# Kernel tuning notes

Measured on AMD Instinct MI355X. Metric: run time of the kernel, lower is better.

## Reference

```python
import jax, jax.numpy as jnp
import numpy as np

TAU = 1.0
NUM_CLASSES = 14
EDGE_W = 500.0
BODY_W = 200.0
LOSS_W = 1.0


def _cross_reduce(x, op, pad_val):
    """Apply op over the 3D 6-neighborhood cross (scipy default structure).
    x: bool [B, C, D, H, W]."""
    p = jnp.pad(x, ((0, 0), (0, 0), (1, 1), (1, 1), (1, 1)), constant_values=pad_val)
    r = p[:, :, 1:-1, 1:-1, 1:-1]
    r = op(r, p[:, :, :-2, 1:-1, 1:-1]); r = op(r, p[:, :, 2:, 1:-1, 1:-1])
    r = op(r, p[:, :, 1:-1, :-2, 1:-1]); r = op(r, p[:, :, 1:-1, 2:, 1:-1])
    r = op(r, p[:, :, 1:-1, 1:-1, :-2]); r = op(r, p[:, :, 1:-1, 1:-1, 2:])
    return r


def _edge_body_masks(gt_labels):
    # gt_labels: int [B, 1, D, H, W] -> bool masks [B, NUM_CLASSES, D, H, W]
    gt = gt_labels[:, 0]  # [B, D, H, W]
    onehot = gt[:, None] == jnp.arange(NUM_CLASSES, dtype=gt.dtype)[None, :, None, None, None]
    # binary_dilation ^ binary_erosion, both with border_value=0 (scipy default)
    dil = _cross_reduce(onehot, jnp.logical_or, False)
    ero = _cross_reduce(onehot, jnp.logical_and, False)
    edges = jnp.logical_xor(dil, ero)
    bodies = jnp.logical_and(jnp.logical_not(edges), onehot)
    # class 0 (background) masks are forced to zero in the original loop
    edges = edges.at[:, 0].set(False)
    bodies = bodies.at[:, 0].set(False)
    return edges, bodies


def _cwd(preds_S, preds_T):
    # ChannelWiseDivergence: per-(batch,channel) softmax over flattened spatial dims
    B, C = preds_S.shape[0], preds_S.shape[1]
    s = preds_S.reshape(B * C, -1) / TAU
    t = preds_T.reshape(B * C, -1) / TAU
    p_t = jax.nn.softmax(t, axis=-1)
    loss = jnp.sum(p_t * (jax.nn.log_softmax(t, axis=-1) - jax.nn.log_softmax(s, axis=-1)))
    return loss * (TAU ** 2) / (B * C)


def setup_inputs() -> dict:
    key = jax.random.key(0)
    k1, k2, k3 = jax.random.split(key, 3)
    B, C, D, H, W = 2, NUM_CLASSES, 96, 96, 96
    preds_S = jax.random.normal(k1, (B, C, D, H, W), dtype=jnp.float32)
    preds_T = jax.random.normal(k2, (B, C, D, H, W), dtype=jnp.float32)
    gt_labels = jax.random.randint(k3, (B, 1, D, H, W), 0, NUM_CLASSES, dtype=jnp.int64)
    return {"preds_S": preds_S, "preds_T": preds_T, "gt_labels": gt_labels}


def reference(preds_S, preds_T, gt_labels):
    B = preds_S.shape[0]
    edges, bodies = _edge_body_masks(gt_labels)
    me = edges.astype(preds_S.dtype)
    mb = bodies.astype(preds_S.dtype)
    loss_edges = _cwd(preds_S * me, preds_T * me) * LOSS_W * EDGE_W / B
    loss_bodies = _cwd(preds_S * mb, preds_T * mb) * LOSS_W * BODY_W / B
    return loss_edges, loss_bodies
```

## Files before the change

kernel.cpp:

```cpp
#include <hip/hip_runtime.h>
#include <math.h>

#define NCLS 14
#define DIMX 96
#define DIMXY (DIMX * DIMX)
#define NVOX (DIMX * DIMX * DIMX)
#define BATCH 2
#define ROWS (BATCH * NCLS)
#define TPB 256
#define VPT 2
#define CPB (TPB * 4 * VPT)
#define NBLK (NVOX / CPB)

__global__ __launch_bounds__(256) void mask_kernel(const int* __restrict__ gt,
                                                   unsigned* __restrict__ masks,
                                                   float* __restrict__ body_acc) {
    if (blockIdx.x == 0 && threadIdx.x < ROWS * 4) body_acc[threadIdx.x] = 0.f;
    int idx4 = blockIdx.x * 256 + threadIdx.x;
    if (idx4 >= BATCH * NVOX / 4) return;
    int v4 = idx4 * 4;
    int b = v4 / NVOX;
    int v = v4 - b * NVOX;
    int w = v % DIMX;
    int h = (v / DIMX) % DIMX;
    int d = v / DIMXY;
    const int* __restrict__ g = gt + (size_t)b * NVOX;

    int gc[4];
    { int4 t4 = *(const int4*)&g[v]; gc[0] = t4.x; gc[1] = t4.y; gc[2] = t4.z; gc[3] = t4.w; }
    bool hasU = h > 0, hasD = h < DIMX - 1, hasF = d > 0, hasB = d < DIMX - 1;
    bool hasL0 = w > 0;
    bool hasR3 = (w + 3) < DIMX - 1;
    int up[4], dn[4], fr[4], bk[4];
    if (hasU) { int4 t4 = *(const int4*)&g[v - DIMX];  up[0]=t4.x; up[1]=t4.y; up[2]=t4.z; up[3]=t4.w; }
    if (hasD) { int4 t4 = *(const int4*)&g[v + DIMX];  dn[0]=t4.x; dn[1]=t4.y; dn[2]=t4.z; dn[3]=t4.w; }
    if (hasF) { int4 t4 = *(const int4*)&g[v - DIMXY]; fr[0]=t4.x; fr[1]=t4.y; fr[2]=t4.z; fr[3]=t4.w; }
    if (hasB) { int4 t4 = *(const int4*)&g[v + DIMXY]; bk[0]=t4.x; bk[1]=t4.y; bk[2]=t4.z; bk[3]=t4.w; }
    int lf0 = hasL0 ? g[v - 1] : 0;
    int rt3 = hasR3 ? g[v + 4] : 0;

    unsigned res[4];
    #pragma unroll
    for (int j = 0; j < 4; ++j) {
        int c0 = gc[j];
        unsigned dil = 1u << c0;
        bool all = hasU && hasD && hasF && hasB;
        int  lf = (j == 0) ? lf0 : gc[j - 1]; bool hl = (j > 0) || hasL0;
        int  rt = (j == 3) ? rt3 : gc[j + 1]; bool hr = (j < 3) || hasR3;
        all = all && hl && hr;
        if (hl)   { dil |= 1u << lf;    all = all && (lf == c0); }
        if (hr)   { dil |= 1u << rt;    all = all && (rt == c0); }
        if (hasU) { dil |= 1u << up[j]; all = all && (up[j] == c0); }
        if (hasD) { dil |= 1u << dn[j]; all = all && (dn[j] == c0); }
        if (hasF) { dil |= 1u << fr[j]; all = all && (fr[j] == c0); }
        if (hasB) { dil |= 1u << bk[j]; all = all && (bk[j] == c0); }
        unsigned edge = dil & ~1u;
        if (all) edge &= ~(1u << c0);
        unsigned bodyc = (all && c0 != 0) ? (unsigned)c0 : 15u;
        res[j] = edge | (bodyc << 16);
    }
    *(uint4*)&masks[(size_t)v4] = make_uint4(res[0], res[1], res[2], res[3]);
}

__global__ __launch_bounds__(TPB) void cwd_kernel(const float* __restrict__ Sp,
                                                  const float* __restrict__ Tp,
                                                  const unsigned* __restrict__ masks,
                                                  float* __restrict__ partials,
                                                  float* __restrict__ body_acc) {
    int blk = blockIdx.x;
    int b = blk / NBLK;
    int chunk = blk - b * NBLK;
    const unsigned* __restrict__ mp = masks + (size_t)b * NVOX;
    const float* __restrict__ tb = Tp + (size_t)b * NCLS * NVOX;
    const float* __restrict__ sb = Sp + (size_t)b * NCLS * NVOX;
    int base = chunk * CPB + (int)threadIdx.x * 4;

    float zt[NCLS], s1[NCLS], zs[NCLS];
    #pragma unroll
    for (int c = 0; c < NCLS; ++c) { zt[c] = 0.f; s1[c] = 0.f; zs[c] = 0.f; }

    #pragma unroll
    for (int k = 0; k < VPT; ++k) {
        int v = base + k * (TPB * 4);
        uint4 wm4 = *(const uint4*)&mp[v];
        unsigned wm[4] = {wm4.x, wm4.y, wm4.z, wm4.w};
        #pragma unroll
        for (int c = 0; c < NCLS; ++c) {
            float4 t4 = *(const float4*)&tb[(size_t)c * NVOX + v];
            float4 s4 = *(const float4*)&sb[(size_t)c * NVOX + v];
            float tt[4] = {t4.x, t4.y, t4.z, t4.w};
            float ss[4] = {s4.x, s4.y, s4.z, s4.w};
            #pragma unroll
            for (int j = 0; j < 4; ++j) {
                float me = (float)((wm[j] >> c) & 1u);
                float tv = tt[j] * me;
                float sv = ss[j] * me;
                float et = __expf(tv);
                zt[c] += et;
                s1[c] += et * (tv - sv);
                zs[c] += __expf(sv);
            }
        }
        #pragma unroll
        for (int j = 0; j < 4; ++j) {
            unsigned bc = wm[j] >> 16;
            if (bc != 15u) {
                size_t off = (size_t)bc * NVOX + (size_t)(v + j);
                float t = tb[off], s = sb[off];
                float* acc = body_acc + ((size_t)b * NCLS + bc) * 4;
                atomicAdd(acc + 0, __expf(t));
                atomicAdd(acc + 1, __expf(t) * (t - s));
                atomicAdd(acc + 2, __expf(s));
                atomicAdd(acc + 3, 1.f);
            }
        }
    }

    #pragma unroll
    for (int off = 32; off > 0; off >>= 1) {
        #pragma unroll
        for (int c = 0; c < NCLS; ++c) {
            zt[c] += __shfl_down(zt[c], off);
            s1[c] += __shfl_down(s1[c], off);
            zs[c] += __shfl_down(zs[c], off);
        }
    }
    __shared__ float red[4][NCLS * 3];
    int wid = (int)threadIdx.x >> 6;
    int lane = (int)threadIdx.x & 63;
    if (lane == 0) {
        #pragma unroll
        for (int c = 0; c < NCLS; ++c) {
            red[wid][c * 3 + 0] = zt[c];
            red[wid][c * 3 + 1] = s1[c];
            red[wid][c * 3 + 2] = zs[c];
        }
    }
    __syncthreads();
    if (threadIdx.x < NCLS * 3) {
        int i = (int)threadIdx.x;
        float s = (red[0][i] + red[1][i]) + (red[2][i] + red[3][i]);
        partials[(size_t)blk * (NCLS * 3) + i] = s;
    }
}

__global__ __launch_bounds__(1024) void final_kernel(const float* __restrict__ partials,
                                                     const float* __restrict__ body_acc,
                                                     float* __restrict__ out) {
    int tid = (int)threadIdx.x;
    int row = tid >> 5;
    int sub = tid & 31;
    __shared__ double les[ROWS], lbs[ROWS];
    if (row < ROWS) {
        int b = row / NCLS, c = row - b * NCLS;
        double zt = 0.0, s1 = 0.0, zs = 0.0;
        for (int k = sub; k < NBLK; k += 32) {
            const float* p = partials + (size_t)(b * NBLK + k) * (NCLS * 3) + c * 3;
            zt += (double)p[0]; s1 += (double)p[1]; zs += (double)p[2];
        }
        #pragma unroll
        for (int off = 16; off > 0; off >>= 1) {
            zt += __shfl_down(zt, off, 32);
            s1 += __shfl_down(s1, off, 32);
            zs += __shfl_down(zs, off, 32);
        }
        if (sub == 0) {
            double le = s1 / zt - log(zt) + log(zs);
            const float* a = body_acc + (size_t)row * 4;
            double rem = (double)NVOX - (double)a[3];
            double bzt = (double)a[0] + rem;
            double bzs = (double)a[2] + rem;
            double lb = (double)a[1] / bzt - log(bzt) + log(bzs);
            les[row] = le;
            lbs[row] = lb;
        }
    }
    __syncthreads();
    if (tid == 0) {
        double A = 0.0, C = 0.0;
        for (int i = 0; i < ROWS; ++i) { A += les[i]; C += lbs[i]; }
        out[0] = (float)(A * (500.0 / 56.0));
        out[1] = (float)(C * (200.0 / 56.0));
    }
}

extern "C" void kernel_launch(void* const* d_in, const int* in_sizes, int n_in,
                              void* d_out, int out_size, void* d_ws, size_t ws_size,
                              hipStream_t stream) {
    const float* Sp = (const float*)d_in[0];
    const float* Tp = (const float*)d_in[1];
    const int* gt = (const int*)d_in[2];
    float* out = (float*)d_out;

    unsigned* masks = (unsigned*)d_ws;
    float* partials = (float*)((char*)d_ws + (size_t)BATCH * NVOX * sizeof(unsigned));
    float* body_acc = partials + (size_t)BATCH * NBLK * (NCLS * 3);

    hipLaunchKernelGGL(mask_kernel, dim3(BATCH * NVOX / 4 / 256), dim3(256), 0, stream,
                       gt, masks, body_acc);
    hipLaunchKernelGGL(cwd_kernel, dim3(BATCH * NBLK), dim3(TPB), 0, stream,
                       Sp, Tp, masks, partials, body_acc);
    hipLaunchKernelGGL(final_kernel, dim3(1), dim3(1024), 0, stream,
                       partials, body_acc, out);
}
```

Baseline: 57.40 us.

## Store edge masks as per-class bit planes and split CWD grid per (batch,class) row

```diff
diff --git a/kernel.cpp b/kernel.cpp
--- a/kernel.cpp
+++ b/kernel.cpp
@@ -5,48 +5,53 @@
 #define DIMX 96
 #define DIMXY (DIMX * DIMX)
 #define NVOX (DIMX * DIMX * DIMX)
+#define NVOX8 (NVOX / 8)
 #define BATCH 2
 #define ROWS (BATCH * NCLS)
 #define TPB 256
-#define VPT 2
-#define CPB (TPB * 4 * VPT)
+#define CPB 4096
 #define NBLK (NVOX / CPB)
 
 __global__ __launch_bounds__(256) void mask_kernel(const int* __restrict__ gt,
-                                                   unsigned* __restrict__ masks,
-                                                   float* __restrict__ body_acc) {
-    if (blockIdx.x == 0 && threadIdx.x < ROWS * 4) body_acc[threadIdx.x] = 0.f;
-    int idx4 = blockIdx.x * 256 + threadIdx.x;
-    if (idx4 >= BATCH * NVOX / 4) return;
-    int v4 = idx4 * 4;
-    int b = v4 / NVOX;
-    int v = v4 - b * NVOX;
+                                                   unsigned char* __restrict__ planes,
+                                                   float* __restrict__ body_acc,
+                                                   const float* __restrict__ Sp,
+                                                   const float* __restrict__ Tp) {
+    int t8 = blockIdx.x * 256 + threadIdx.x;
+    if (t8 >= BATCH * NVOX8) return;
+    int b = t8 / NVOX8;
+    int lb = t8 - b * NVOX8;
+    int v = lb * 8;
     int w = v % DIMX;
     int h = (v / DIMX) % DIMX;
     int d = v / DIMXY;
     const int* __restrict__ g = gt + (size_t)b * NVOX;
 
-    int gc[4];
-    { int4 t4 = *(const int4*)&g[v]; gc[0] = t4.x; gc[1] = t4.y; gc[2] = t4.z; gc[3] = t4.w; }
+    int gc[8], up[8], dn[8], fr[8], bk[8];
+    { int4 a = *(const int4*)&g[v];     int4 c2 = *(const int4*)&g[v + 4];
+      gc[0]=a.x; gc[1]=a.y; gc[2]=a.z; gc[3]=a.w; gc[4]=c2.x; gc[5]=c2.y; gc[6]=c2.z; gc[7]=c2.w; }
     bool hasU = h > 0, hasD = h < DIMX - 1, hasF = d > 0, hasB = d < DIMX - 1;
     bool hasL0 = w > 0;
-    bool hasR3 = (w + 3) < DIMX - 1;
-    int up[4], dn[4], fr[4], bk[4];
-    if (hasU) { int4 t4 = *(const int4*)&g[v - DIMX];  up[0]=t4.x; up[1]=t4.y; up[2]=t4.z; up[3]=t4.w; }
-    if (hasD) { int4 t4 = *(const int4*)&g[v + DIMX];  dn[0]=t4.x; dn[1]=t4.y; dn[2]=t4.z; dn[3]=t4.w; }
-    if (hasF) { int4 t4 = *(const int4*)&g[v - DIMXY]; fr[0]=t4.x; fr[1]=t4.y; fr[2]=t4.z; fr[3]=t4.w; }
-    if (hasB) { int4 t4 = *(const int4*)&g[v + DIMXY]; bk[0]=t4.x; bk[1]=t4.y; bk[2]=t4.z; bk[3]=t4.w; }
+    bool hasR7 = w < DIMX - 8;
+    if (hasU) { int4 a = *(const int4*)&g[v - DIMX];     int4 c2 = *(const int4*)&g[v - DIMX + 4];
+      up[0]=a.x; up[1]=a.y; up[2]=a.z; up[3]=a.w; up[4]=c2.x; up[5]=c2.y; up[6]=c2.z; up[7]=c2.w; }
+    if (hasD) { int4 a = *(const int4*)&g[v + DIMX];     int4 c2 = *(const int4*)&g[v + DIMX + 4];
+      dn[0]=a.x; dn[1]=a.y; dn[2]=a.z; dn[3]=a.w; dn[4]=c2.x; dn[5]=c2.y; dn[6]=c2.z; dn[7]=c2.w; }
+    if (hasF) { int4 a = *(const int4*)&g[v - DIMXY];    int4 c2 = *(const int4*)&g[v - DIMXY + 4];
+      fr[0]=a.x; fr[1]=a.y; fr[2]=a.z; fr[3]=a.w; fr[4]=c2.x; fr[5]=c2.y; fr[6]=c2.z; fr[7]=c2.w; }
+    if (hasB) { int4 a = *(const int4*)&g[v + DIMXY];    int4 c2 = *(const int4*)&g[v + DIMXY + 4];
+      bk[0]=a.x; bk[1]=a.y; bk[2]=a.z; bk[3]=a.w; bk[4]=c2.x; bk[5]=c2.y; bk[6]=c2.z; bk[7]=c2.w; }
     int lf0 = hasL0 ? g[v - 1] : 0;
-    int rt3 = hasR3 ? g[v + 4] : 0;
-
-    unsigned res[4];
-    #pragma unroll
-    for (int j = 0; j < 4; ++j) {
+    int rt7 = hasR7 ? g[v + 8] : 0;
+
+    unsigned e[8];
+    #pragma unroll
+    for (int j = 0; j < 8; ++j) {
         int c0 = gc[j];
         unsigned dil = 1u << c0;
         bool all = hasU && hasD && hasF && hasB;
         int  lf = (j == 0) ? lf0 : gc[j - 1]; bool hl = (j > 0) || hasL0;
-        int  rt = (j == 3) ? rt3 : gc[j + 1]; bool hr = (j < 3) || hasR3;
+        int  rt = (j == 7) ? rt7 : gc[j + 1]; bool hr = (j < 7) || hasR7;
         all = all && hl && hr;
         if (hl)   { dil |= 1u << lf;    all = all && (lf == c0); }
         if (hr)   { dil |= 1u << rt;    all = all && (rt == c0); }
@@ -56,91 +61,91 @@
         if (hasB) { dil |= 1u << bk[j]; all = all && (bk[j] == c0); }
         unsigned edge = dil & ~1u;
         if (all) edge &= ~(1u << c0);
-        unsigned bodyc = (all && c0 != 0) ? (unsigned)c0 : 15u;
-        res[j] = edge | (bodyc << 16);
-    }
-    *(uint4*)&masks[(size_t)v4] = make_uint4(res[0], res[1], res[2], res[3]);
+        e[j] = edge;
+        if (all && c0 != 0) {
+            size_t off = ((size_t)(b * NCLS + c0)) * NVOX + (size_t)(v + j);
+            float t = Tp[off], s = Sp[off];
+            float et = __expf(t);
+            float* acc = body_acc + (size_t)(b * NCLS + c0) * 4;
+            atomicAdd(acc + 0, et);
+            atomicAdd(acc + 1, et * (t - s));
+            atomicAdd(acc + 2, __expf(s));
+            atomicAdd(acc + 3, 1.f);
+        }
+    }
+    #pragma unroll
+    for (int c = 0; c < NCLS; ++c) {
+        unsigned byte = 0;
+        #pragma unroll
+        for (int j = 0; j < 8; ++j) byte |= ((e[j] >> c) & 1u) << j;
+        planes[(size_t)(b * NCLS + c) * NVOX8 + lb] = (unsigned char)byte;
+    }
 }
 
 __global__ __launch_bounds__(TPB) void cwd_kernel(const float* __restrict__ Sp,
                                                   const float* __restrict__ Tp,
-                                                  const unsigned* __restrict__ masks,
-                                                  float* __restrict__ partials,
-                                                  float* __restrict__ body_acc) {
+                                                  const unsigned char* __restrict__ planes,
+                                                  float* __restrict__ partials) {
     int blk = blockIdx.x;
-    int b = blk / NBLK;
-    int chunk = blk - b * NBLK;
-    const unsigned* __restrict__ mp = masks + (size_t)b * NVOX;
-    const float* __restrict__ tb = Tp + (size_t)b * NCLS * NVOX;
-    const float* __restrict__ sb = Sp + (size_t)b * NCLS * NVOX;
-    int base = chunk * CPB + (int)threadIdx.x * 4;
-
-    float zt[NCLS], s1[NCLS], zs[NCLS];
-    #pragma unroll
-    for (int c = 0; c < NCLS; ++c) { zt[c] = 0.f; s1[c] = 0.f; zs[c] = 0.f; }
-
-    #pragma unroll
-    for (int k = 0; k < VPT; ++k) {
-        int v = base + k * (TPB * 4);
-        uint4 wm4 = *(const uint4*)&mp[v];
-        unsigned wm[4] = {wm4.x, wm4.y, wm4.z, wm4.w};
-        #pragma unroll
-        for (int c = 0; c < NCLS; ++c) {
-            float4 t4 = *(const float4*)&tb[(size_t)c * NVOX + v];
-            float4 s4 = *(const float4*)&sb[(size_t)c * NVOX + v];
-            float tt[4] = {t4.x, t4.y, t4.z, t4.w};
-            float ss[4] = {s4.x, s4.y, s4.z, s4.w};
-            #pragma unroll
-            for (int j = 0; j < 4; ++j) {
-                float me = (float)((wm[j] >> c) & 1u);
-                float tv = tt[j] * me;
-                float sv = ss[j] * me;
-                float et = __expf(tv);
-                zt[c] += et;
-                s1[c] += et * (tv - sv);
-                zs[c] += __expf(sv);
-            }
-        }
+    int row = blk / NBLK;
+    int chunk = blk - row * NBLK;
+    const float* __restrict__ tp = Tp + (size_t)row * NVOX;
+    const float* __restrict__ sp = Sp + (size_t)row * NVOX;
+    const unsigned char* __restrict__ pl = planes + (size_t)row * NVOX8;
+    int tid = (int)threadIdx.x;
+    int v0 = chunk * CPB + tid * 8;
+    int bidx = chunk * (CPB / 8) + tid;
+
+    unsigned m0 = pl[bidx];
+    unsigned m1 = pl[bidx + TPB];
+    unsigned mword = m0 | (m1 << 8);
+
+    float zt[4] = {0.f, 0.f, 0.f, 0.f};
+    float s1[4] = {0.f, 0.f, 0.f, 0.f};
+    float zs[4] = {0.f, 0.f, 0.f, 0.f};
+
+    float4 tc = *(const float4*)&tp[v0];
+    float4 sc = *(const float4*)&sp[v0];
+    #pragma unroll
+    for (int g = 0; g < 4; ++g) {
+        float4 tn, sn;
+        if (g < 3) {
+            int an = v0 + ((g + 1) >> 1) * 2048 + (((g + 1) & 1) << 2);
+            tn = *(const float4*)&tp[an];
+            sn = *(const float4*)&sp[an];
+        }
+        float tt[4] = {tc.x, tc.y, tc.z, tc.w};
+        float ss[4] = {sc.x, sc.y, sc.z, sc.w};
         #pragma unroll
         for (int j = 0; j < 4; ++j) {
-            unsigned bc = wm[j] >> 16;
-            if (bc != 15u) {
-                size_t off = (size_t)bc * NVOX + (size_t)(v + j);
-                float t = tb[off], s = sb[off];
-                float* acc = body_acc + ((size_t)b * NCLS + bc) * 4;
-                atomicAdd(acc + 0, __expf(t));
-                atomicAdd(acc + 1, __expf(t) * (t - s));
-                atomicAdd(acc + 2, __expf(s));
-                atomicAdd(acc + 3, 1.f);
-            }
-        }
-    }
-
+            float me = (float)((mword >> (g * 4 + j)) & 1u);
+            float tv = tt[j] * me;
+            float sv = ss[j] * me;
+            float et = __expf(tv);
+            zt[j] += et;
+            s1[j] += et * (tv - sv);
+            zs[j] += __expf(sv);
+        }
+        tc = tn; sc = sn;
+    }
+
+    float r0 = (zt[0] + zt[1]) + (zt[2] + zt[3]);
+    float r1 = (s1[0] + s1[1]) + (s1[2] + s1[3]);
+    float r2 = (zs[0] + zs[1]) + (zs[2] + zs[3]);
     #pragma unroll
     for (int off = 32; off > 0; off >>= 1) {
-        #pragma unroll
-        for (int c = 0; c < NCLS; ++c) {
-            zt[c] += __shfl_down(zt[c], off);
-            s1[c] += __shfl_down(s1[c], off);
-            zs[c] += __shfl_down(zs[c], off);
-        }
-    }
-    __shared__ float red[4][NCLS * 3];
-    int wid = (int)threadIdx.x >> 6;
-    int lane = (int)threadIdx.x & 63;
-    if (lane == 0) {
-        #pragma unroll
-        for (int c = 0; c < NCLS; ++c) {
-            red[wid][c * 3 + 0] = zt[c];
-            red[wid][c * 3 + 1] = s1[c];
-            red[wid][c * 3 + 2] = zs[c];
-        }
-    }
+        r0 += __shfl_down(r0, off);
+        r1 += __shfl_down(r1, off);
+        r2 += __shfl_down(r2, off);
+    }
+    __shared__ float red[4][3];
+    int wid = tid >> 6;
+    int lane = tid & 63;
+    if (lane == 0) { red[wid][0] = r0; red[wid][1] = r1; red[wid][2] = r2; }
     __syncthreads();
-    if (threadIdx.x < NCLS * 3) {
-        int i = (int)threadIdx.x;
-        float s = (red[0][i] + red[1][i]) + (red[2][i] + red[3][i]);
-        partials[(size_t)blk * (NCLS * 3) + i] = s;
+    if (tid < 3) {
+        partials[(size_t)blk * 4 + tid] =
+            (red[0][tid] + red[1][tid]) + (red[2][tid] + red[3][tid]);
     }
 }
 
@@ -152,10 +157,9 @@
     int sub = tid & 31;
     __shared__ double les[ROWS], lbs[ROWS];
     if (row < ROWS) {
-        int b = row / NCLS, c = row - b * NCLS;
         double zt = 0.0, s1 = 0.0, zs = 0.0;
         for (int k = sub; k < NBLK; k += 32) {
-            const float* p = partials + (size_t)(b * NBLK + k) * (NCLS * 3) + c * 3;
+            const float* p = partials + (size_t)(row * NBLK + k) * 4;
             zt += (double)p[0]; s1 += (double)p[1]; zs += (double)p[2];
         }
         #pragma unroll
@@ -192,14 +196,15 @@
     const int* gt = (const int*)d_in[2];
     float* out = (float*)d_out;
 
-    unsigned* masks = (unsigned*)d_ws;
-    float* partials = (float*)((char*)d_ws + (size_t)BATCH * NVOX * sizeof(unsigned));
-    float* body_acc = partials + (size_t)BATCH * NBLK * (NCLS * 3);
-
-    hipLaunchKernelGGL(mask_kernel, dim3(BATCH * NVOX / 4 / 256), dim3(256), 0, stream,
-                       gt, masks, body_acc);
-    hipLaunchKernelGGL(cwd_kernel, dim3(BATCH * NBLK), dim3(TPB), 0, stream,
-                       Sp, Tp, masks, partials, body_acc);
+    unsigned char* planes = (unsigned char*)d_ws;
+    float* partials = (float*)((char*)d_ws + (size_t)ROWS * NVOX8);
+    float* body_acc = partials + (size_t)ROWS * NBLK * 4;
+
+    hipMemsetAsync(body_acc, 0, ROWS * 4 * sizeof(float), stream);
+    hipLaunchKernelGGL(mask_kernel, dim3((BATCH * NVOX8 + 255) / 256), dim3(256), 0, stream,
+                       gt, planes, body_acc, Sp, Tp);
+    hipLaunchKernelGGL(cwd_kernel, dim3(ROWS * NBLK), dim3(TPB), 0, stream,
+                       Sp, Tp, planes, partials);
     hipLaunchKernelGGL(final_kernel, dim3(1), dim3(1024), 0, stream,
                        partials, body_acc, out);
 }
```

Result: faster. 55.04 us (-4.1%).
